# Optimization experiments

Hardware: AMD Instinct MI355X
Metric: run time of the kernel (lower is better)

## Reference

```python
import jax, jax.numpy as jnp
import numpy as np

S, DM, H, DH, FF, L = 2048, 1024, 16, 64, 4096, 2
N_IMG, GH, GW = 4, 16, 32  # 4 images, each 16x32=512 tokens
THETA = 10000.0
LN_EPS = 1e-5


def _rope_tables():
    # 2D repeated rope: dim=DH, dim//4 freqs, x/y angles interleaved -> DH//2 per token
    fr = 1.0 / THETA ** (np.arange(0, DH, 4)[: DH // 4] / DH)  # [DH//4]
    pos = np.arange(GH * GW)
    xang = np.outer(pos % GW, fr)   # [512, DH//4]
    yang = np.outer(pos // GW, fr)  # [512, DH//4]
    ang = np.stack([xang, yang], axis=-1).reshape(GH * GW, DH // 2)  # [512, DH//2]
    ang = np.tile(ang, (N_IMG, 1))  # same grid repeated per image -> [S, DH//2]
    return np.cos(ang).astype(np.float32), np.sin(ang).astype(np.float32)


def setup_inputs() -> dict:
    key = jax.random.key(0)
    ks = jax.random.split(key, 8)
    scale = 0.02

    def rn(k, shape):
        return jax.random.normal(k, shape, jnp.float32) * scale

    x = jax.random.normal(ks[0], (S, DM), jnp.float32)
    input_row_offsets = jnp.array([0, 512, 1024, 1536, 2048], jnp.int32)
    cos_np, sin_np = _rope_tables()
    inp = {
        "x": x,
        "input_row_offsets": input_row_offsets,
        "freqs_cos": jnp.asarray(cos_np),
        "freqs_sin": jnp.asarray(sin_np),
        # stacked per-layer params [L, ...]; Linear weights stored as [in, out]
        "ln0_g": jnp.ones((L, DM), jnp.float32),
        "ln0_b": jnp.zeros((L, DM), jnp.float32),
        "ln1_g": jnp.ones((L, DM), jnp.float32),
        "ln1_b": jnp.zeros((L, DM), jnp.float32),
        "wqkv_w": rn(ks[1], (L, DM, 3 * DM)),
        "wqkv_b": jnp.zeros((L, 3 * DM), jnp.float32),
        "wo_w": rn(ks[2], (L, DM, DM)),
        "wo_b": jnp.zeros((L, DM), jnp.float32),
        "up_w": rn(ks[3], (L, DM, FF)),
        "up_b": jnp.zeros((L, FF), jnp.float32),
        "down_w": rn(ks[4], (L, FF, DM)),
        "down_b": jnp.zeros((L, DM), jnp.float32),
        "lnf_g": jnp.ones((DM,), jnp.float32),
        "lnf_b": jnp.zeros((DM,), jnp.float32),
    }
    return inp


def _layernorm(v, g, b):
    m = v.mean(-1, keepdims=True)
    var = v.var(-1, keepdims=True)
    return (v - m) * jax.lax.rsqrt(var + LN_EPS) * g + b


def _rope(t, cos, sin):
    # t: [S, H, DH]; pairs (even, odd) rotated by complex freqs (broadcast over heads)
    tr = t.reshape(S, H, DH // 2, 2)
    te, to = tr[..., 0], tr[..., 1]
    c = cos[:, None, :]
    s = sin[:, None, :]
    oe = te * c - to * s
    oo = te * s + to * c
    return jnp.stack([oe, oo], axis=-1).reshape(S, H, DH)


def reference(x, input_row_offsets, freqs_cos, freqs_sin,
              ln0_g, ln0_b, ln1_g, ln1_b, wqkv_w, wqkv_b, wo_w, wo_b,
              up_w, up_b, down_w, down_b, lnf_g, lnf_b):
    # Block-diagonal mask. NOTE: the torch reference ADDS the boolean mask
    # (True -> +1.0) to the logits, it does NOT mask with -inf. Replicated faithfully.
    seg = jnp.searchsorted(input_row_offsets, jnp.arange(S), side="right")
    maskf = (seg[:, None] == seg[None, :]).astype(jnp.float32)  # [S, S]
    inv_sqrt_d = 1.0 / jnp.sqrt(jnp.float32(DH))

    def layer(h, p):
        g0, b0, g1, b1, Wqkv, bqkv, Wo, bo, Wu, bu, Wd, bd = p
        y = _layernorm(h, g0, b0)
        qkv = (y @ Wqkv + bqkv).reshape(S, 3, H, DH)
        q, k, v = qkv[:, 0], qkv[:, 1], qkv[:, 2]
        q = _rope(q, freqs_cos, freqs_sin)
        k = _rope(k, freqs_cos, freqs_sin)
        aw = jnp.einsum("shd,thd->hst", q, k) * inv_sqrt_d + maskf[None]  # [H,S,S]
        aw = jax.nn.softmax(aw.astype(jnp.float32), axis=-1).astype(q.dtype)
        ao = jnp.einsum("hst,thd->shd", aw, v).reshape(S, DM)
        h = h + ao @ Wo + bo
        y = _layernorm(h, g1, b1)
        y = jax.nn.gelu(y @ Wu + bu, approximate=True)
        h = h + y @ Wd + bd
        return h, None

    params = (ln0_g, ln0_b, ln1_g, ln1_b, wqkv_w, wqkv_b, wo_w, wo_b,
              up_w, up_b, down_w, down_b)
    h, _ = jax.lax.scan(layer, x, params)
    return _layernorm(h, lnf_g, lnf_b)
```

## Files before the change

### kernel.cpp

```cpp
#include <hip/hip_runtime.h>
#include <hip/hip_bf16.h>
#include <stdint.h>
#include <math.h>

#define S_LEN 2048
#define DMODEL 1024
#define NHEAD 16
#define DHEAD 64
#define FFDIM 4096
#define NLAYER 2

using bf16 = __hip_bfloat16;
typedef __attribute__((ext_vector_type(8))) short bf16x8;
typedef __attribute__((ext_vector_type(4))) float f32x4;
typedef __attribute__((ext_vector_type(16))) float f32x16;
typedef __attribute__((ext_vector_type(4))) int i32x4;

#define MFMA16x16(A, B, C) __builtin_amdgcn_mfma_f32_16x16x32_bf16(A, B, C, 0, 0, 0)
#define MFMA32x32(A, B, C) __builtin_amdgcn_mfma_f32_32x32x16_bf16(A, B, C, 0, 0, 0)
#define EXP2(x) __builtin_amdgcn_exp2f(x)

__device__ __forceinline__ float bf2f(uint32_t u16bits) {
  union { uint32_t i; float f; } x;
  x.i = u16bits << 16;
  return x.f;
}
__device__ __forceinline__ uint16_t f2bf(float f) {
  return __builtin_bit_cast(uint16_t, __float2bfloat16(f));
}

__device__ __forceinline__ uint32_t cvtpk(float lo, float hi) {
  uint32_t r;
  asm("v_cvt_pk_bf16_f32 %0, %1, %2" : "=v"(r) : "v"(lo), "v"(hi));
  return r;
}
__device__ __forceinline__ void pl32swap(uint32_t& a, uint32_t& b) {
#if __has_builtin(__builtin_amdgcn_permlane32_swap)
  typedef __attribute__((ext_vector_type(2))) int i32x2;
  i32x2 r = __builtin_amdgcn_permlane32_swap((int)a, (int)b, false, false);
  a = (uint32_t)r.x;
  b = (uint32_t)r.y;
#else
  asm volatile("v_permlane32_swap_b32 %0, %1" : "+v"(a), "+v"(b));
#endif
}

__global__ __launch_bounds__(256) void k_tcast(const float* __restrict__ in,
                                               bf16* __restrict__ out,
                                               int R, int C) {
  __shared__ float tl[32][33];
  int t = threadIdx.x;
  int r0 = blockIdx.y * 32, c0 = blockIdx.x * 32;
  int cl = t & 31, rl = t >> 5;
#pragma unroll
  for (int i = 0; i < 4; ++i)
    tl[rl + i * 8][cl] = in[(size_t)(r0 + rl + i * 8) * C + c0 + cl];
  __syncthreads();
#pragma unroll
  for (int i = 0; i < 4; ++i)
    out[(size_t)(c0 + rl + i * 8) * R + r0 + cl] = __float2bfloat16(tl[cl][rl + i * 8]);
}

__device__ __forceinline__ void ln_store4(bf16* p, float a, float b, float c, float d) {
  uint2 u;
  u.x = (uint32_t)f2bf(a) | ((uint32_t)f2bf(b) << 16);
  u.y = (uint32_t)f2bf(c) | ((uint32_t)f2bf(d) << 16);
  *(uint2*)p = u;
}
__device__ __forceinline__ void ln_store4(float* p, float a, float b, float c, float d) {
  *(float4*)p = make_float4(a, b, c, d);
}

template <typename OUT>
__global__ __launch_bounds__(256) void k_ln(const float* __restrict__ h,
                                            const float* __restrict__ g,
                                            const float* __restrict__ b,
                                            OUT* __restrict__ y) {
  int row = blockIdx.x, t = threadIdx.x;
  const float4 v = ((const float4*)(h + (size_t)row * DMODEL))[t];
  float s = v.x + v.y + v.z + v.w;
  float s2 = v.x * v.x + v.y * v.y + v.z * v.z + v.w * v.w;
#pragma unroll
  for (int off = 32; off > 0; off >>= 1) {
    s += __shfl_down(s, off);
    s2 += __shfl_down(s2, off);
  }
  __shared__ float red[8];
  int w = t >> 6;
  if ((t & 63) == 0) { red[w] = s; red[4 + w] = s2; }
  __syncthreads();
  s = red[0] + red[1] + red[2] + red[3];
  s2 = red[4] + red[5] + red[6] + red[7];
  float mean = s * (1.0f / DMODEL);
  float var = s2 * (1.0f / DMODEL) - mean * mean;
  float rstd = rsqrtf(var + 1e-5f);
  float4 gv = ((const float4*)g)[t];
  float4 bv = ((const float4*)b)[t];
  float o0 = (v.x - mean) * rstd * gv.x + bv.x;
  float o1 = (v.y - mean) * rstd * gv.y + bv.y;
  float o2 = (v.z - mean) * rstd * gv.z + bv.z;
  float o3 = (v.w - mean) * rstd * gv.w + bv.w;
  ln_store4(y + (size_t)row * DMODEL + t * 4, o0, o1, o2, o3);
}

__global__ __launch_bounds__(256) void k_rope(const bf16* __restrict__ qkv,
                                              const float* __restrict__ fcos,
                                              const float* __restrict__ fsin,
                                              bf16* __restrict__ qr,
                                              bf16* __restrict__ kr) {
  int idx = blockIdx.x * 256 + threadIdx.x;
  int p = idx & 31;
  int hh = (idx >> 5) & (NHEAD - 1);
  int s = idx >> 9;
  float c = fcos[s * 32 + p], sn = fsin[s * 32 + p];
  int colq = hh * DHEAD + 2 * p;
  uint32_t rq = *(const uint32_t*)(qkv + (size_t)s * 3 * DMODEL + colq);
  uint32_t rk = *(const uint32_t*)(qkv + (size_t)s * 3 * DMODEL + DMODEL + colq);
  {
    float te = bf2f(rq & 0xffffu), to = bf2f(rq >> 16);
    uint32_t outv = (uint32_t)f2bf(te * c - to * sn) | ((uint32_t)f2bf(te * sn + to * c) << 16);
    *(uint32_t*)(qr + (size_t)s * DMODEL + colq) = outv;
  }
  {
    float te = bf2f(rk & 0xffffu), to = bf2f(rk >> 16);
    uint32_t outv = (uint32_t)f2bf(te * c - to * sn) | ((uint32_t)f2bf(te * sn + to * c) << 16);
    *(uint32_t*)(kr + (size_t)s * DMODEL + colq) = outv;
  }
}

__global__ __launch_bounds__(256) void k_tv(const bf16* __restrict__ qkv,
                                            bf16* __restrict__ vT) {
  __shared__ bf16 tl[64][65];
  int t = threadIdx.x;
  int hh = blockIdx.y;
  int sb = blockIdx.x * 64;
#pragma unroll
  for (int i = 0; i < 16; ++i) {
    int e = i * 256 + t;
    int sl = e >> 6, d = e & 63;
    tl[sl][d] = qkv[(size_t)(sb + sl) * 3 * DMODEL + 2 * DMODEL + hh * DHEAD + d];
  }
  __syncthreads();
#pragma unroll
  for (int i = 0; i < 16; ++i) {
    int e = i * 256 + t;
    int d = e >> 6, sl = e & 63;
    vT[(size_t)(hh * DHEAD + d) * S_LEN + sb + sl] = tl[sl][d];
  }
}

template <int EPI, int BM>
__global__ __launch_bounds__(256) void k_gemm2(const bf16* __restrict__ A,
                                               const bf16* __restrict__ BT,
                                               const float* __restrict__ bias,
                                               void* __restrict__ out,
                                               int M, int N, int K, int Kc) {
  constexpr int MF = BM / 32;
  __shared__ bf16 As[2][BM * 64];
  __shared__ bf16 Bs[2][128 * 64];
  int t = threadIdx.x;
  int w = t >> 6, l = t & 63, lr = l & 15, lg = l >> 4;

  int nxy = gridDim.x * gridDim.y;
  int bid = blockIdx.y * gridDim.x + blockIdx.x;
  int chk8 = nxy >> 3;
  int swz = (bid & 7) * chk8 + (bid >> 3);
  int bx = swz % gridDim.x, by = swz / gridDim.x;
  int bm = bx * BM, bn = by * 128;
  int k0 = blockIdx.z * Kc;
  int wm = (w >> 1) * (BM / 2), wn = (w & 1) * 64;

  f32x4 zero4 = {0.f, 0.f, 0.f, 0.f};
  f32x4 acc[MF][4];
#pragma unroll
  for (int mf = 0; mf < MF; ++mf)
#pragma unroll
    for (int nf = 0; nf < 4; ++nf) acc[mf][nf] = zero4;

  auto stage = [&](int buf, int kk) {
#pragma unroll
    for (int i = 0; i < BM / 32; ++i) {
      int chunk = i * 256 + t;
      int row = chunk >> 3;
      int scol = ((chunk ^ row) & 7) << 3;
      __builtin_amdgcn_global_load_lds(
          (__attribute__((address_space(1))) void*)(A + (size_t)(bm + row) * K + kk + scol),
          (__attribute__((address_space(3))) void*)(&As[buf][chunk * 8]), 16, 0, 0);
    }
#pragma unroll
    for (int i = 0; i < 4; ++i) {
      int chunk = i * 256 + t;
      int row = chunk >> 3;
      int scol = ((chunk ^ row) & 7) << 3;
      __builtin_amdgcn_global_load_lds(
          (__attribute__((address_space(1))) void*)(BT + (size_t)(bn + row) * K + kk + scol),
          (__attribute__((address_space(3))) void*)(&Bs[buf][chunk * 8]), 16, 0, 0);
    }
  };

  int nt = Kc / 64;
  stage(0, k0);
  __syncthreads();
  int cur = 0;
  for (int kt = 0; kt < nt; ++kt) {
    bf16x8 af[2][MF], bfr[2][4];
#pragma unroll
    for (int h = 0; h < 2; ++h) {
#pragma unroll
      for (int mf = 0; mf < MF; ++mf) {
        int row = wm + mf * 16 + lr;
        af[h][mf] = *(const bf16x8*)(&As[cur][row * 64 + ((((h << 2) + lg) ^ (row & 7)) << 3)]);
      }
#pragma unroll
      for (int nf = 0; nf < 4; ++nf) {
        int row = wn + nf * 16 + lr;
        bfr[h][nf] = *(const bf16x8*)(&Bs[cur][row * 64 + ((((h << 2) + lg) ^ (row & 7)) << 3)]);
      }
    }
    __builtin_amdgcn_sched_barrier(0);
    if (kt + 1 < nt) stage(cur ^ 1, k0 + (kt + 1) * 64);
    __builtin_amdgcn_sched_barrier(0);
#pragma unroll
    for (int h = 0; h < 2; ++h)
#pragma unroll
      for (int mf = 0; mf < MF; ++mf)
#pragma unroll
        for (int nf = 0; nf < 4; ++nf)
          acc[mf][nf] = MFMA16x16(af[h][mf], bfr[h][nf], acc[mf][nf]);
    __syncthreads();
    cur ^= 1;
  }

  if (EPI == 3) {
    float* outf = (float*)out + (size_t)blockIdx.z * ((size_t)M * N);
#pragma unroll
    for (int mf = 0; mf < MF; ++mf)
#pragma unroll
      for (int nf = 0; nf < 4; ++nf) {
        int col = bn + wn + nf * 16 + lr;
        int row0 = bm + wm + mf * 16 + lg * 4;
#pragma unroll
        for (int r = 0; r < 4; ++r)
          outf[(size_t)(row0 + r) * N + col] = acc[mf][nf][r];
      }
  } else {
    bf16* outb = (bf16*)out;
#pragma unroll
    for (int mf = 0; mf < MF; ++mf)
#pragma unroll
      for (int nf = 0; nf < 4; ++nf) {
        int col = bn + wn + nf * 16 + lr;
        float bv = bias[col];
        int row0 = bm + wm + mf * 16 + lg * 4;
#pragma unroll
        for (int r = 0; r < 4; ++r) {
          float v = acc[mf][nf][r] + bv;
          if (EPI == 2)
            v = 0.5f * v * (1.0f + tanhf(0.7978845608028654f * (v + 0.044715f * v * v * v)));
          outb[(size_t)(row0 + r) * N + col] = __float2bfloat16(v);
        }
      }
  }
}

template <int KS>
__global__ __launch_bounds__(256) void k_reduce(const float* __restrict__ part,
                                                const float* __restrict__ bias,
                                                float* __restrict__ hb,
                                                int MN, int N) {
  int i4 = (blockIdx.x * 256 + threadIdx.x) * 4;
  float4 r = *(const float4*)(hb + i4);
  float4 b = *(const float4*)(bias + (i4 & (N - 1)));
  float sx = r.x + b.x, sy = r.y + b.y, sz = r.z + b.z, sw = r.w + b.w;
#pragma unroll
  for (int ks = 0; ks < KS; ++ks) {
    float4 p = *(const float4*)(part + (size_t)ks * MN + i4);
    sx += p.x; sy += p.y; sz += p.z; sw += p.w;
  }
  *(float4*)(hb + i4) = make_float4(sx, sy, sz, sw);
}

#define ATTN_TILE(KC0, KC1, KC2, KC3, KN0, KN1, KN2, KN3, IT)                  \
  {                                                                            \
    const int j0 = jbase + (IT) * 32;                                          \
    f32x16 sC;                                                                 \
    _Pragma("unroll") for (int r = 0; r < 16; ++r) sC[r] = 0.f;                \
    __builtin_amdgcn_s_setprio(1);                                             \
    sC = MFMA32x32(KC0, qf0, sC);                                              \
    sC = MFMA32x32(KC1, qf1, sC);                                              \
    sC = MFMA32x32(KC2, qf2, sC);                                              \
    sC = MFMA32x32(KC3, qf3, sC);                                              \
    __builtin_amdgcn_s_setprio(0);                                             \
    const bf16* vbase = vrow + j0;                                             \
    bf16x8 va00 = *(const bf16x8*)(vbase);                                     \
    bf16x8 va01 = *(const bf16x8*)(vbase + 16);                                \
    bf16x8 va10 = *(const bf16x8*)(vbase + 32 * S_LEN);                        \
    bf16x8 va11 = *(const bf16x8*)(vbase + 32 * S_LEN + 16);                   \
    {                                                                          \
      int jn = j0 + 32;                                                        \
      int jmax = jbase + 480;                                                  \
      jn = (jn > jmax) ? jmax : jn;                                            \
      const bf16* kn = krow + (size_t)jn * DMODEL;                             \
      KN0 = *(const bf16x8*)(kn);                                              \
      KN1 = *(const bf16x8*)(kn + 16);                                         \
      KN2 = *(const bf16x8*)(kn + 32);                                         \
      KN3 = *(const bf16x8*)(kn + 48);                                         \
    }                                                                          \
    int tt = j0 + hi * 4 - sl0;                                                \
    _Pragma("unroll") for (int r = 0; r < 16; ++r) {                           \
      int ku = tt + ((r & 3) + 8 * (r >> 2));                                  \
      float fb = ((uint32_t)ku < spanu) ? LOG2E : 0.0f;                        \
      sC[r] = sC[r] * C1 + fb;                                                 \
    }                                                                          \
    float rm = sC[0];                                                          \
    _Pragma("unroll") for (int r = 1; r < 16; ++r) rm = fmaxf(rm, sC[r]);      \
    uint32_t ra = __builtin_bit_cast(uint32_t, rm), rb = ra;                   \
    pl32swap(ra, rb);                                                          \
    float rmax =                                                               \
        fmaxf(__builtin_bit_cast(float, ra), __builtin_bit_cast(float, rb));   \
    if (__any(rmax > m_r + 8.0f)) {                                            \
      float mn = fmaxf(m_r, rmax);                                             \
      float fs = EXP2(m_r - mn);                                               \
      m_r = mn;                                                                \
      l_r *= fs;                                                               \
      _Pragma("unroll") for (int r = 0; r < 16; ++r) {                         \
        oC0[r] *= fs;                                                          \
        oC1[r] *= fs;                                                          \
      }                                                                        \
    }                                                                          \
    _Pragma("unroll") for (int r = 0; r < 16; ++r) {                           \
      float pv = EXP2(sC[r] - m_r);                                            \
      sC[r] = pv;                                                              \
      l_r += pv;                                                               \
    }                                                                          \
    uint32_t u0 = cvtpk(sC[0], sC[1]), u1 = cvtpk(sC[2], sC[3]);               \
    uint32_t u2 = cvtpk(sC[4], sC[5]), u3 = cvtpk(sC[6], sC[7]);               \
    uint32_t u4 = cvtpk(sC[8], sC[9]), u5 = cvtpk(sC[10], sC[11]);             \
    uint32_t u6 = cvtpk(sC[12], sC[13]), u7 = cvtpk(sC[14], sC[15]);           \
    pl32swap(u0, u2);                                                          \
    pl32swap(u1, u3);                                                          \
    pl32swap(u4, u6);                                                          \
    pl32swap(u5, u7);                                                          \
    i32x4 pi0 = {(int)u0, (int)u1, (int)u2, (int)u3};                          \
    i32x4 pi1 = {(int)u4, (int)u5, (int)u6, (int)u7};                          \
    bf16x8 pb0 = __builtin_bit_cast(bf16x8, pi0);                              \
    bf16x8 pb1 = __builtin_bit_cast(bf16x8, pi1);                              \
    __builtin_amdgcn_s_setprio(1);                                             \
    oC0 = MFMA32x32(va00, pb0, oC0);                                           \
    oC0 = MFMA32x32(va01, pb1, oC0);                                           \
    oC1 = MFMA32x32(va10, pb0, oC1);                                           \
    oC1 = MFMA32x32(va11, pb1, oC1);                                           \
    __builtin_amdgcn_s_setprio(0);                                             \
  }

__global__ __launch_bounds__(256, 3) void k_attn(const bf16* __restrict__ qr,
                                                 const bf16* __restrict__ kr,
                                                 const bf16* __restrict__ vT,
                                                 const int* __restrict__ offs,
                                                 bf16* __restrict__ ao) {
  __shared__ float oO[4][64][33];
  __shared__ float mM[4][32];
  __shared__ float lL[4][32];

  int t = threadIdx.x, w = t >> 6, l = t & 63;
  int ql = l & 31, hi = l >> 5, hi8 = hi * 8;
  int hh = blockIdx.x, qb = blockIdx.y * 32;
  int h64 = hh * DHEAD;

  constexpr float LOG2E = 1.4426950408889634f;
  constexpr float C1 = 0.125f * LOG2E;

  int q = qb + ql;
  int o0 = offs[0], o1 = offs[1], o2 = offs[2], o3 = offs[3], o4 = offs[4];
  int sl0 = -1073741824, sh0 = 1073741824;
  sl0 = (o0 <= q) ? o0 : sl0;
  sl0 = (o1 <= q) ? o1 : sl0;
  sl0 = (o2 <= q) ? o2 : sl0;
  sl0 = (o3 <= q) ? o3 : sl0;
  sl0 = (o4 <= q) ? o4 : sl0;
  sh0 = (o4 > q) ? o4 : sh0;
  sh0 = (o3 > q) ? o3 : sh0;
  sh0 = (o2 > q) ? o2 : sh0;
  sh0 = (o1 > q) ? o1 : sh0;
  sh0 = (o0 > q) ? o0 : sh0;
  uint32_t spanu = (uint32_t)(sh0 - sl0);

  const bf16* qbase = qr + (size_t)q * DMODEL + h64 + hi8;
  bf16x8 qf0 = *(const bf16x8*)(qbase);
  bf16x8 qf1 = *(const bf16x8*)(qbase + 16);
  bf16x8 qf2 = *(const bf16x8*)(qbase + 32);
  bf16x8 qf3 = *(const bf16x8*)(qbase + 48);

  f32x16 oC0, oC1;
#pragma unroll
  for (int r = 0; r < 16; ++r) { oC0[r] = 0.f; oC1[r] = 0.f; }
  float m_r = -1e30f, l_r = 0.f;

  const bf16* vrow = vT + (size_t)(h64 + ql) * S_LEN + hi8;
  const bf16* krow = kr + (size_t)ql * DMODEL + h64 + hi8;
  int jbase = w * 512;

  bf16x8 kA0, kA1, kA2, kA3, kB0, kB1, kB2, kB3;
  {
    const bf16* kb = krow + (size_t)jbase * DMODEL;
    kA0 = *(const bf16x8*)(kb);
    kA1 = *(const bf16x8*)(kb + 16);
    kA2 = *(const bf16x8*)(kb + 32);
    kA3 = *(const bf16x8*)(kb + 48);
  }

  for (int itp = 0; itp < 8; ++itp) {
    ATTN_TILE(kA0, kA1, kA2, kA3, kB0, kB1, kB2, kB3, itp * 2);
    ATTN_TILE(kB0, kB1, kB2, kB3, kA0, kA1, kA2, kA3, itp * 2 + 1);
  }

  {
    uint32_t la = __builtin_bit_cast(uint32_t, l_r), lb = la;
    pl32swap(la, lb);
    l_r = __builtin_bit_cast(float, la) + __builtin_bit_cast(float, lb);
  }
  if (hi == 0) {
    mM[w][ql] = m_r;
    lL[w][ql] = l_r;
  }
#pragma unroll
  for (int r = 0; r < 16; ++r) {
    int d = (r & 3) + 8 * (r >> 2) + 4 * hi;
    oO[w][d][ql] = oC0[r];
    oO[w][d + 32][ql] = oC1[r];
  }
  __syncthreads();

  {
    int mq = t & 31, dbse = (t >> 5) * 8;
    float m0 = mM[0][mq], m1 = mM[1][mq], m2 = mM[2][mq], m3 = mM[3][mq];
    float ms = fmaxf(fmaxf(m0, m1), fmaxf(m2, m3));
    float a0 = EXP2(m0 - ms), a1 = EXP2(m1 - ms), a2 = EXP2(m2 - ms), a3 = EXP2(m3 - ms);
    float ll = a0 * lL[0][mq] + a1 * lL[1][mq] + a2 * lL[2][mq] + a3 * lL[3][mq];
    float inv = 1.0f / ll;
    uint4 pkv;
    uint32_t pw[4];
#pragma unroll
    for (int i = 0; i < 4; ++i) {
      int d0 = dbse + 2 * i, d1 = dbse + 2 * i + 1;
      float e0 = (a0 * oO[0][d0][mq] + a1 * oO[1][d0][mq] + a2 * oO[2][d0][mq] +
                  a3 * oO[3][d0][mq]) * inv;
      float e1 = (a0 * oO[0][d1][mq] + a1 * oO[1][d1][mq] + a2 * oO[2][d1][mq] +
                  a3 * oO[3][d1][mq]) * inv;
      pw[i] = (uint32_t)f2bf(e0) | ((uint32_t)f2bf(e1) << 16);
    }
    pkv.x = pw[0]; pkv.y = pw[1]; pkv.z = pw[2]; pkv.w = pw[3];
    *(uint4*)(ao + (size_t)(qb + mq) * DMODEL + h64 + dbse) = pkv;
  }
}

extern "C" void kernel_launch(void* const* d_in, const int* in_sizes, int n_in,
                              void* d_out, int out_size, void* d_ws, size_t ws_size,
                              hipStream_t stream) {
  const float* x = (const float*)d_in[0];
  const int* offs = (const int*)d_in[1];
  const float* fcos = (const float*)d_in[2];
  const float* fsin = (const float*)d_in[3];
  const float* ln0g = (const float*)d_in[4];
  const float* ln0b = (const float*)d_in[5];
  const float* ln1g = (const float*)d_in[6];
  const float* ln1b = (const float*)d_in[7];
  const float* wqkv = (const float*)d_in[8];
  const float* bqkv = (const float*)d_in[9];
  const float* wo = (const float*)d_in[10];
  const float* bo = (const float*)d_in[11];
  const float* wu = (const float*)d_in[12];
  const float* bu = (const float*)d_in[13];
  const float* wd = (const float*)d_in[14];
  const float* bd = (const float*)d_in[15];
  const float* lnfg = (const float*)d_in[16];
  const float* lnfb = (const float*)d_in[17];

  char* ws = (char*)d_ws;
  size_t off = 0;
  auto alloc = [&](size_t bytes) -> void* {
    void* p = ws + off;
    off += (bytes + 255) & ~(size_t)255;
    return p;
  };
  bf16* wqkvT = (bf16*)alloc((size_t)NLAYER * 3 * DMODEL * DMODEL * 2);
  bf16* woT = (bf16*)alloc((size_t)NLAYER * DMODEL * DMODEL * 2);
  bf16* wuT = (bf16*)alloc((size_t)NLAYER * DMODEL * FFDIM * 2);
  bf16* wdT = (bf16*)alloc((size_t)NLAYER * FFDIM * DMODEL * 2);
  float* hbuf = (float*)alloc((size_t)S_LEN * DMODEL * 4);
  bf16* ybuf = (bf16*)alloc((size_t)S_LEN * DMODEL * 2);
  bf16* qkv = (bf16*)alloc((size_t)S_LEN * 3 * DMODEL * 2);
  bf16* qrb = (bf16*)alloc((size_t)S_LEN * DMODEL * 2);
  bf16* krb = (bf16*)alloc((size_t)S_LEN * DMODEL * 2);
  bf16* vTb = (bf16*)alloc((size_t)S_LEN * DMODEL * 2);
  bf16* aob = (bf16*)alloc((size_t)S_LEN * DMODEL * 2);
  bf16* midb = (bf16*)alloc((size_t)S_LEN * FFDIM * 2);

  float* partWO = (float*)qkv;
  float* partDN = (float*)ybuf;

  for (int ly = 0; ly < NLAYER; ++ly) {
    k_tcast<<<dim3(3 * DMODEL / 32, DMODEL / 32), 256, 0, stream>>>(
        wqkv + (size_t)ly * DMODEL * 3 * DMODEL, wqkvT + (size_t)ly * 3 * DMODEL * DMODEL, DMODEL, 3 * DMODEL);
    k_tcast<<<dim3(DMODEL / 32, DMODEL / 32), 256, 0, stream>>>(
        wo + (size_t)ly * DMODEL * DMODEL, woT + (size_t)ly * DMODEL * DMODEL, DMODEL, DMODEL);
    k_tcast<<<dim3(FFDIM / 32, DMODEL / 32), 256, 0, stream>>>(
        wu + (size_t)ly * DMODEL * FFDIM, wuT + (size_t)ly * DMODEL * FFDIM, DMODEL, FFDIM);
    k_tcast<<<dim3(DMODEL / 32, FFDIM / 32), 256, 0, stream>>>(
        wd + (size_t)ly * FFDIM * DMODEL, wdT + (size_t)ly * FFDIM * DMODEL, FFDIM, DMODEL);
  }
  hipMemcpyAsync(hbuf, x, (size_t)S_LEN * DMODEL * 4, hipMemcpyDeviceToDevice, stream);

  for (int ly = 0; ly < NLAYER; ++ly) {
    k_ln<bf16><<<S_LEN, 256, 0, stream>>>(hbuf, ln0g + ly * DMODEL, ln0b + ly * DMODEL, ybuf);
    k_gemm2<0, 128><<<dim3(S_LEN / 128, 3 * DMODEL / 128, 1), 256, 0, stream>>>(
        ybuf, wqkvT + (size_t)ly * 3 * DMODEL * DMODEL, bqkv + ly * 3 * DMODEL, qkv,
        S_LEN, 3 * DMODEL, DMODEL, DMODEL);
    k_rope<<<S_LEN * NHEAD * 32 / 256, 256, 0, stream>>>(qkv, fcos, fsin, qrb, krb);
    k_tv<<<dim3(S_LEN / 64, NHEAD), 256, 0, stream>>>(qkv, vTb);
    k_attn<<<dim3(NHEAD, S_LEN / 32), 256, 0, stream>>>(qrb, krb, vTb, offs, aob);
    k_gemm2<3, 64><<<dim3(S_LEN / 64, DMODEL / 128, 2), 256, 0, stream>>>(
        aob, woT + (size_t)ly * DMODEL * DMODEL, nullptr, partWO,
        S_LEN, DMODEL, DMODEL, DMODEL / 2);
    k_reduce<2><<<S_LEN * DMODEL / 1024, 256, 0, stream>>>(
        partWO, bo + ly * DMODEL, hbuf, S_LEN * DMODEL, DMODEL);
    k_ln<bf16><<<S_LEN, 256, 0, stream>>>(hbuf, ln1g + ly * DMODEL, ln1b + ly * DMODEL, ybuf);
    k_gemm2<2, 128><<<dim3(S_LEN / 128, FFDIM / 128, 1), 256, 0, stream>>>(
        ybuf, wuT + (size_t)ly * DMODEL * FFDIM, bu + ly * FFDIM, midb,
        S_LEN, FFDIM, DMODEL, DMODEL);
    k_gemm2<3, 128><<<dim3(S_LEN / 128, DMODEL / 128, 4), 256, 0, stream>>>(
        midb, wdT + (size_t)ly * FFDIM * DMODEL, nullptr, partDN,
        S_LEN, DMODEL, FFDIM, FFDIM / 4);
    k_reduce<4><<<S_LEN * DMODEL / 1024, 256, 0, stream>>>(
        partDN, bd + ly * DMODEL, hbuf, S_LEN * DMODEL, DMODEL);
  }
  k_ln<float><<<S_LEN, 256, 0, stream>>>(hbuf, lnfg, lnfb, (float*)d_out);
}
```

Before: 408.4 us.

## Fuse split-K reduce with layernorm, merge rope and V transpose, raise attn occupancy

The split-K partial-sum reduction and residual add are now fused with the following layernorm in one row-wise kernel, so the separate reduce and LN launches become one. The RoPE kernel and the V-transpose kernel are merged into a single launch. A separate ybuf2 is added because ybuf is aliased as the down-projection partial buffer. The attention kernel's launch bounds go from 3 to 4 blocks per SM, which may force register spills.

```diff
diff --git a/kernel.cpp b/kernel.cpp
--- a/kernel.cpp
+++ b/kernel.cpp
@@ -72,14 +72,12 @@
 }
 
 template <typename OUT>
-__global__ __launch_bounds__(256) void k_ln(const float* __restrict__ h,
-                                            const float* __restrict__ g,
-                                            const float* __restrict__ b,
-                                            OUT* __restrict__ y) {
-  int row = blockIdx.x, t = threadIdx.x;
-  const float4 v = ((const float4*)(h + (size_t)row * DMODEL))[t];
-  float s = v.x + v.y + v.z + v.w;
-  float s2 = v.x * v.x + v.y * v.y + v.z * v.z + v.w * v.w;
+__device__ __forceinline__ void ln_rowcore(float v0, float v1, float v2, float v3,
+                                           const float* __restrict__ g,
+                                           const float* __restrict__ b,
+                                           OUT* __restrict__ yrow, int t) {
+  float s = v0 + v1 + v2 + v3;
+  float s2 = v0 * v0 + v1 * v1 + v2 * v2 + v3 * v3;
 #pragma unroll
   for (int off = 32; off > 0; off >>= 1) {
     s += __shfl_down(s, off);
@@ -96,44 +94,72 @@
   float rstd = rsqrtf(var + 1e-5f);
   float4 gv = ((const float4*)g)[t];
   float4 bv = ((const float4*)b)[t];
-  float o0 = (v.x - mean) * rstd * gv.x + bv.x;
-  float o1 = (v.y - mean) * rstd * gv.y + bv.y;
-  float o2 = (v.z - mean) * rstd * gv.z + bv.z;
-  float o3 = (v.w - mean) * rstd * gv.w + bv.w;
-  ln_store4(y + (size_t)row * DMODEL + t * 4, o0, o1, o2, o3);
-}
-
-__global__ __launch_bounds__(256) void k_rope(const bf16* __restrict__ qkv,
-                                              const float* __restrict__ fcos,
-                                              const float* __restrict__ fsin,
-                                              bf16* __restrict__ qr,
-                                              bf16* __restrict__ kr) {
-  int idx = blockIdx.x * 256 + threadIdx.x;
-  int p = idx & 31;
-  int hh = (idx >> 5) & (NHEAD - 1);
-  int s = idx >> 9;
-  float c = fcos[s * 32 + p], sn = fsin[s * 32 + p];
-  int colq = hh * DHEAD + 2 * p;
-  uint32_t rq = *(const uint32_t*)(qkv + (size_t)s * 3 * DMODEL + colq);
-  uint32_t rk = *(const uint32_t*)(qkv + (size_t)s * 3 * DMODEL + DMODEL + colq);
-  {
-    float te = bf2f(rq & 0xffffu), to = bf2f(rq >> 16);
-    uint32_t outv = (uint32_t)f2bf(te * c - to * sn) | ((uint32_t)f2bf(te * sn + to * c) << 16);
-    *(uint32_t*)(qr + (size_t)s * DMODEL + colq) = outv;
-  }
-  {
-    float te = bf2f(rk & 0xffffu), to = bf2f(rk >> 16);
-    uint32_t outv = (uint32_t)f2bf(te * c - to * sn) | ((uint32_t)f2bf(te * sn + to * c) << 16);
-    *(uint32_t*)(kr + (size_t)s * DMODEL + colq) = outv;
-  }
-}
-
-__global__ __launch_bounds__(256) void k_tv(const bf16* __restrict__ qkv,
-                                            bf16* __restrict__ vT) {
+  ln_store4(yrow + t * 4, (v0 - mean) * rstd * gv.x + bv.x,
+            (v1 - mean) * rstd * gv.y + bv.y, (v2 - mean) * rstd * gv.z + bv.z,
+            (v3 - mean) * rstd * gv.w + bv.w);
+}
+
+template <typename OUT>
+__global__ __launch_bounds__(256) void k_ln(const float* __restrict__ h,
+                                            const float* __restrict__ g,
+                                            const float* __restrict__ b,
+                                            OUT* __restrict__ y) {
+  int row = blockIdx.x, t = threadIdx.x;
+  const float4 v = ((const float4*)(h + (size_t)row * DMODEL))[t];
+  ln_rowcore<OUT>(v.x, v.y, v.z, v.w, g, b, y + (size_t)row * DMODEL, t);
+}
+
+template <int KS, typename OUT>
+__global__ __launch_bounds__(256) void k_redln(const float* __restrict__ part,
+                                               const float* __restrict__ bias,
+                                               float* __restrict__ hb,
+                                               const float* __restrict__ g,
+                                               const float* __restrict__ b,
+                                               OUT* __restrict__ y) {
+  int row = blockIdx.x, t = threadIdx.x;
+  size_t base = (size_t)row * DMODEL + t * 4;
+  float4 r = *(const float4*)(hb + base);
+  float4 bv = *(const float4*)(bias + t * 4);
+  float v0 = r.x + bv.x, v1 = r.y + bv.y, v2 = r.z + bv.z, v3 = r.w + bv.w;
+#pragma unroll
+  for (int ks = 0; ks < KS; ++ks) {
+    float4 p = *(const float4*)(part + (size_t)ks * (S_LEN * DMODEL) + base);
+    v0 += p.x; v1 += p.y; v2 += p.z; v3 += p.w;
+  }
+  *(float4*)(hb + base) = make_float4(v0, v1, v2, v3);
+  ln_rowcore<OUT>(v0, v1, v2, v3, g, b, y + (size_t)row * DMODEL, t);
+}
+
+__global__ __launch_bounds__(256) void k_ropetv(const bf16* __restrict__ qkv,
+                                                const float* __restrict__ fcos,
+                                                const float* __restrict__ fsin,
+                                                bf16* __restrict__ qr,
+                                                bf16* __restrict__ kr,
+                                                bf16* __restrict__ vT) {
   __shared__ bf16 tl[64][65];
   int t = threadIdx.x;
   int hh = blockIdx.y;
   int sb = blockIdx.x * 64;
+#pragma unroll
+  for (int i = 0; i < 8; ++i) {
+    int e = i * 256 + t;
+    int p = e & 31, sl = e >> 5;
+    int s = sb + sl;
+    float c = fcos[s * 32 + p], sn = fsin[s * 32 + p];
+    int colq = hh * DHEAD + 2 * p;
+    uint32_t rq = *(const uint32_t*)(qkv + (size_t)s * 3 * DMODEL + colq);
+    uint32_t rk = *(const uint32_t*)(qkv + (size_t)s * 3 * DMODEL + DMODEL + colq);
+    {
+      float te = bf2f(rq & 0xffffu), to = bf2f(rq >> 16);
+      uint32_t outv = (uint32_t)f2bf(te * c - to * sn) | ((uint32_t)f2bf(te * sn + to * c) << 16);
+      *(uint32_t*)(qr + (size_t)s * DMODEL + colq) = outv;
+    }
+    {
+      float te = bf2f(rk & 0xffffu), to = bf2f(rk >> 16);
+      uint32_t outv = (uint32_t)f2bf(te * c - to * sn) | ((uint32_t)f2bf(te * sn + to * c) << 16);
+      *(uint32_t*)(kr + (size_t)s * DMODEL + colq) = outv;
+    }
+  }
 #pragma unroll
   for (int i = 0; i < 16; ++i) {
     int e = i * 256 + t;
@@ -261,23 +287,6 @@
         }
       }
   }
-}
-
-template <int KS>
-__global__ __launch_bounds__(256) void k_reduce(const float* __restrict__ part,
-                                                const float* __restrict__ bias,
-                                                float* __restrict__ hb,
-                                                int MN, int N) {
-  int i4 = (blockIdx.x * 256 + threadIdx.x) * 4;
-  float4 r = *(const float4*)(hb + i4);
-  float4 b = *(const float4*)(bias + (i4 & (N - 1)));
-  float sx = r.x + b.x, sy = r.y + b.y, sz = r.z + b.z, sw = r.w + b.w;
-#pragma unroll
-  for (int ks = 0; ks < KS; ++ks) {
-    float4 p = *(const float4*)(part + (size_t)ks * MN + i4);
-    sx += p.x; sy += p.y; sz += p.z; sw += p.w;
-  }
-  *(float4*)(hb + i4) = make_float4(sx, sy, sz, sw);
 }
 
 #define ATTN_TILE(KC0, KC1, KC2, KC3, KN0, KN1, KN2, KN3, IT)                  \
@@ -353,7 +362,7 @@
     __builtin_amdgcn_s_setprio(0);                                             \
   }
 
-__global__ __launch_bounds__(256, 3) void k_attn(const bf16* __restrict__ qr,
+__global__ __launch_bounds__(256, 4) void k_attn(const bf16* __restrict__ qr,
                                                  const bf16* __restrict__ kr,
                                                  const bf16* __restrict__ vT,
                                                  const int* __restrict__ offs,
@@ -495,6 +504,7 @@
   bf16* vTb = (bf16*)alloc((size_t)S_LEN * DMODEL * 2);
   bf16* aob = (bf16*)alloc((size_t)S_LEN * DMODEL * 2);
   bf16* midb = (bf16*)alloc((size_t)S_LEN * FFDIM * 2);
+  bf16* ybuf2 = (bf16*)alloc((size_t)S_LEN * DMODEL * 2);
 
   float* partWO = (float*)qkv;
   float* partDN = (float*)ybuf;
@@ -511,28 +521,32 @@
   }
   hipMemcpyAsync(hbuf, x, (size_t)S_LEN * DMODEL * 4, hipMemcpyDeviceToDevice, stream);
 
+  k_ln<bf16><<<S_LEN, 256, 0, stream>>>(hbuf, ln0g, ln0b, ybuf2);
+
   for (int ly = 0; ly < NLAYER; ++ly) {
-    k_ln<bf16><<<S_LEN, 256, 0, stream>>>(hbuf, ln0g + ly * DMODEL, ln0b + ly * DMODEL, ybuf);
     k_gemm2<0, 128><<<dim3(S_LEN / 128, 3 * DMODEL / 128, 1), 256, 0, stream>>>(
-        ybuf, wqkvT + (size_t)ly * 3 * DMODEL * DMODEL, bqkv + ly * 3 * DMODEL, qkv,
+        ybuf2, wqkvT + (size_t)ly * 3 * DMODEL * DMODEL, bqkv + ly * 3 * DMODEL, qkv,
         S_LEN, 3 * DMODEL, DMODEL, DMODEL);
-    k_rope<<<S_LEN * NHEAD * 32 / 256, 256, 0, stream>>>(qkv, fcos, fsin, qrb, krb);
-    k_tv<<<dim3(S_LEN / 64, NHEAD), 256, 0, stream>>>(qkv, vTb);
+    k_ropetv<<<dim3(S_LEN / 64, NHEAD), 256, 0, stream>>>(qkv, fcos, fsin, qrb, krb, vTb);
     k_attn<<<dim3(NHEAD, S_LEN / 32), 256, 0, stream>>>(qrb, krb, vTb, offs, aob);
     k_gemm2<3, 64><<<dim3(S_LEN / 64, DMODEL / 128, 2), 256, 0, stream>>>(
         aob, woT + (size_t)ly * DMODEL * DMODEL, nullptr, partWO,
         S_LEN, DMODEL, DMODEL, DMODEL / 2);
-    k_reduce<2><<<S_LEN * DMODEL / 1024, 256, 0, stream>>>(
-        partWO, bo + ly * DMODEL, hbuf, S_LEN * DMODEL, DMODEL);
-    k_ln<bf16><<<S_LEN, 256, 0, stream>>>(hbuf, ln1g + ly * DMODEL, ln1b + ly * DMODEL, ybuf);
+    k_redln<2, bf16><<<S_LEN, 256, 0, stream>>>(
+        partWO, bo + ly * DMODEL, hbuf, ln1g + ly * DMODEL, ln1b + ly * DMODEL, ybuf2);
     k_gemm2<2, 128><<<dim3(S_LEN / 128, FFDIM / 128, 1), 256, 0, stream>>>(
-        ybuf, wuT + (size_t)ly * DMODEL * FFDIM, bu + ly * FFDIM, midb,
+        ybuf2, wuT + (size_t)ly * DMODEL * FFDIM, bu + ly * FFDIM, midb,
         S_LEN, FFDIM, DMODEL, DMODEL);
     k_gemm2<3, 128><<<dim3(S_LEN / 128, DMODEL / 128, 4), 256, 0, stream>>>(
         midb, wdT + (size_t)ly * FFDIM * DMODEL, nullptr, partDN,
         S_LEN, DMODEL, FFDIM, FFDIM / 4);
-    k_reduce<4><<<S_LEN * DMODEL / 1024, 256, 0, stream>>>(
-        partDN, bd + ly * DMODEL, hbuf, S_LEN * DMODEL, DMODEL);
-  }
-  k_ln<float><<<S_LEN, 256, 0, stream>>>(hbuf, lnfg, lnfb, (float*)d_out);
-}
+    if (ly + 1 < NLAYER) {
+      k_redln<4, bf16><<<S_LEN, 256, 0, stream>>>(
+          partDN, bd + ly * DMODEL, hbuf, ln0g + (ly + 1) * DMODEL,
+          ln0b + (ly + 1) * DMODEL, ybuf2);
+    } else {
+      k_redln<4, float><<<S_LEN, 256, 0, stream>>>(
+          partDN, bd + ly * DMODEL, hbuf, lnfg, lnfb, (float*)d_out);
+    }
+  }
+}
```

After: 393.5 us. -3.7%, faster.
